# Performance work log

Measured on AMD Instinct MI355X. Metric: run time of the kernel, lower is better.

Reference implementation:

```python
import jax, jax.numpy as jnp
import numpy as np
import math

D_MODEL = 512
N_HEAD = 8
D_K = D_MODEL // N_HEAD
BN_EPS = 1e-5


def setup_inputs() -> dict:
    key = jax.random.key(0)
    ks = jax.random.split(key, 24)
    B, L = 4, 2048
    s = 0.02
    inp = {
        'query': jax.random.normal(ks[0], (B, L, D_MODEL), jnp.float32),
        'key':   jax.random.normal(ks[1], (B, L, D_MODEL), jnp.float32),
        'value': jax.random.normal(ks[2], (B, L, D_MODEL), jnp.float32),
        # multi-scale conv (kernel sizes 3 and 5)
        'conv_w3': jax.random.normal(ks[3], (D_MODEL, D_MODEL, 3), jnp.float32) * s,
        'conv_b3': jnp.zeros((D_MODEL,), jnp.float32),
        'conv_w5': jax.random.normal(ks[4], (D_MODEL, D_MODEL, 5), jnp.float32) * s,
        'conv_b5': jnp.zeros((D_MODEL,), jnp.float32),
        # batchnorm over 2*d_model channels (inference mode, running stats)
        'bn_gamma': jnp.ones((2 * D_MODEL,), jnp.float32),
        'bn_beta':  jnp.zeros((2 * D_MODEL,), jnp.float32),
        'bn_mean':  jnp.zeros((2 * D_MODEL,), jnp.float32),
        'bn_var':   jnp.ones((2 * D_MODEL,), jnp.float32),
        # linear projections (torch layout: [out, in])
        'wq':  jax.random.normal(ks[5], (D_MODEL, D_MODEL), jnp.float32) * s,
        'bq':  jnp.zeros((D_MODEL,), jnp.float32),
        'wkl': jax.random.normal(ks[6], (D_MODEL, 2 * D_MODEL), jnp.float32) * s,
        'bkl': jnp.zeros((D_MODEL,), jnp.float32),
        'wkg': jax.random.normal(ks[7], (D_MODEL, D_MODEL), jnp.float32) * s,
        'bkg': jnp.zeros((D_MODEL,), jnp.float32),
        'wv':  jax.random.normal(ks[8], (D_MODEL, D_MODEL), jnp.float32) * s,
        'bv':  jnp.zeros((D_MODEL,), jnp.float32),
        'wo':  jax.random.normal(ks[9], (D_MODEL, D_MODEL), jnp.float32) * s,
        'bo':  jnp.zeros((D_MODEL,), jnp.float32),
    }
    return inp


def _conv1d_same(x_ncl, w_oik, b, pad):
    # x: [B, C_in, L], w: [C_out, C_in, K]
    y = jax.lax.conv_general_dilated(
        x_ncl, w_oik, window_strides=(1,), padding=[(pad, pad)],
        dimension_numbers=('NCH', 'OIH', 'NCH'))
    return y + b[None, :, None]


def _heads(x, B, L):
    # [B, L, D] -> [B, L, H, d_k]
    return x.reshape(B, L, N_HEAD, D_K)


def reference(query, key, value, conv_w3, conv_b3, conv_w5, conv_b5,
              bn_gamma, bn_beta, bn_mean, bn_var,
              wq, bq, wkl, bkl, wkg, bkg, wv, bv, wo, bo):
    B, L, _ = query.shape
    # local key path: multi-scale conv over sequence dim
    k_ncl = key.transpose(0, 2, 1)                      # [B, D, L]
    c3 = _conv1d_same(k_ncl, conv_w3, conv_b3, 1)       # [B, D, L]
    c5 = _conv1d_same(k_ncl, conv_w5, conv_b5, 2)       # [B, D, L]
    cat = jnp.concatenate([c3, c5], axis=1)             # [B, 2D, L]
    bn = (cat - bn_mean[None, :, None]) * (bn_gamma[None, :, None]
          * jax.lax.rsqrt(bn_var[None, :, None] + BN_EPS)) + bn_beta[None, :, None]
    key_local = bn.transpose(0, 2, 1)                   # [B, L, 2D]

    q  = _heads(query @ wq.T + bq, B, L)                # [B, L, H, dk]
    kl = _heads(key_local @ wkl.T + bkl, B, L)
    kg = _heads(key @ wkg.T + bkg, B, L)
    v  = _heads(value @ wv.T + bv, B, L)

    scale = 1.0 / math.sqrt(D_K)
    s_loc = jnp.einsum('bqhd,bkhd->bhqk', q, kl) * scale
    s_glo = jnp.einsum('bqhd,bkhd->bhqk', q, kg) * scale
    a_loc = jax.nn.softmax(s_loc, axis=-1)
    a_glo = jax.nn.softmax(s_glo, axis=-1)
    x = jnp.einsum('bhqk,bkhd->bqhd', a_loc, v) + jnp.einsum('bhqk,bkhd->bqhd', a_glo, v)
    x = x.reshape(B, L, N_HEAD * D_K)
    return x @ wo.T + bo
```

## Files before the change

### kernel.cpp

```cpp
#include <hip/hip_runtime.h>
#include <hip/hip_bf16.h>

#define D_MODEL 512
#define SEQ_L   2048
#define NBATCH  4
#define BLROWS  8192
#define BN_EPS_F 1e-5f
#define QK_SCALE 0.18033688011112042f

typedef __attribute__((ext_vector_type(8))) short bf16x8;
typedef __attribute__((ext_vector_type(4))) float f32x4;
typedef __attribute__((ext_vector_type(16))) float f32x16;
typedef __attribute__((ext_vector_type(2))) int i32x2;

__device__ __forceinline__ unsigned short f2bf(float f){
  union { float f; unsigned u; } x; x.f = f;
  return (unsigned short)((x.u + 0x7fffu + ((x.u >> 16) & 1u)) >> 16);
}
__device__ __forceinline__ unsigned pack2bf(float a, float b){
  return (unsigned)f2bf(a) | ((unsigned)f2bf(b) << 16);
}
__device__ __forceinline__ unsigned cvt_pk(float a, float b){
  unsigned r;
  asm("v_cvt_pk_bf16_f32 %0, %1, %2" : "=v"(r) : "v"(a), "v"(b));
  return r;
}
__device__ __forceinline__ float exp2fast(float x){
  float r;
  asm("v_exp_f32 %0, %1" : "=v"(r) : "v"(x));
  return r;
}
__device__ __forceinline__ f32x4 mfma16(bf16x8 a, bf16x8 b, f32x4 c){
  return __builtin_amdgcn_mfma_f32_16x16x32_bf16(a, b, c, 0, 0, 0);
}
__device__ __forceinline__ f32x16 mfma32(bf16x8 a, bf16x8 b, f32x16 c){
  return __builtin_amdgcn_mfma_f32_32x32x16_bf16(a, b, c, 0, 0, 0);
}
__device__ __forceinline__ bf16x8 ldb8(const unsigned short* p){
  return *reinterpret_cast<const bf16x8*>(p);
}
__device__ __forceinline__ void gld16(const void* g, void* l){
  __builtin_amdgcn_global_load_lds(
      (const __attribute__((address_space(1))) unsigned*)g,
      (__attribute__((address_space(3))) unsigned*)l, 16, 0, 0);
}

__global__ void k_prep(
    const float* __restrict__ query, const float* __restrict__ key,
    const float* __restrict__ value,
    const float* __restrict__ wq, const float* __restrict__ wkg,
    const float* __restrict__ wv, const float* __restrict__ wo,
    const float* __restrict__ wkl, const float* __restrict__ gamma,
    const float* __restrict__ beta, const float* __restrict__ mean,
    const float* __restrict__ var, const float* __restrict__ cb3,
    const float* __restrict__ cb5, const float* __restrict__ w3,
    const float* __restrict__ w5, const float* __restrict__ bkl,
    unsigned short* __restrict__ qb, unsigned short* __restrict__ kb,
    unsigned short* __restrict__ vb,
    unsigned short* __restrict__ wqb, unsigned short* __restrict__ wkgb,
    unsigned short* __restrict__ wvb, unsigned short* __restrict__ wob,
    unsigned short* __restrict__ Acat, unsigned short* __restrict__ Bcat,
    float* __restrict__ beff, unsigned short* __restrict__ zeros)
{
  const int blk = blockIdx.x, tid = threadIdx.x;
  if (blk < 12288){
    const int z = blk >> 12, bb = blk & 4095;
    const float* s = (z == 0) ? query : (z == 1) ? key : value;
    unsigned short* d = (z == 0) ? qb : (z == 1) ? kb : vb;
    int i = (bb * 256 + tid) * 4;
    float4 v = *reinterpret_cast<const float4*>(s + i);
    uint2 o; o.x = pack2bf(v.x, v.y); o.y = pack2bf(v.z, v.w);
    *reinterpret_cast<uint2*>(d + i) = o;
  } else if (blk < 13312){
    const int r = blk - 12288, z = r >> 8, bb = r & 255;
    const float* s = (z == 0) ? wq : (z == 1) ? wkg : (z == 2) ? wv : wo;
    unsigned short* d = (z == 0) ? wqb : (z == 1) ? wkgb : (z == 2) ? wvb : wob;
    const float sc = (z == 0) ? QK_SCALE : 1.f;
    int i = (bb * 256 + tid) * 4;
    float4 v = *reinterpret_cast<const float4*>(s + i);
    uint2 o; o.x = pack2bf(v.x * sc, v.y * sc); o.y = pack2bf(v.z * sc, v.w * sc);
    *reinterpret_cast<uint2*>(d + i) = o;
  } else if (blk < 13824){
    int base = (blk - 13312) * 1024 + tid * 4;
    ushort4 out;
#pragma unroll
    for (int j = 0; j < 4; ++j){
      int idx = base + j;
      int o = idx >> 10, ch = idx & 1023;
      int c = (ch < 512) ? (512 + ch) : (ch - 512);
      float a = gamma[c] * rsqrtf(var[c] + BN_EPS_F);
      ((unsigned short*)&out)[j] = f2bf(wkl[o * 1024 + c] * a);
    }
    *reinterpret_cast<ushort4*>(Acat + base) = out;
  } else if (blk < 16384){
    int base = (blk - 13824) * 1024 + tid * 4;
    ushort4 out;
#pragma unroll
    for (int j = 0; j < 4; ++j){
      int idx = base + j;
      int t = idx >> 19; int r = idx & 524287;
      int ci = r >> 10, ch = r & 1023;
      float v;
      if (ch < 512) v = w5[ch * 2560 + ci * 5 + t];
      else {
        int c3 = ch - 512;
        v = (t >= 1 && t <= 3) ? w3[c3 * 1536 + ci * 3 + (t - 1)] : 0.0f;
      }
      ((unsigned short*)&out)[j] = f2bf(v);
    }
    *reinterpret_cast<ushort4*>(Bcat + base) = out;
  } else if (blk < 16512){
    const int o = (blk - 16384) * 4 + (tid >> 6);
    const int lane = tid & 63;
    float acc = 0.f;
    for (int c = lane; c < 1024; c += 64){
      float a = gamma[c] * rsqrtf(var[c] + BN_EPS_F);
      float cb = (c < 512) ? cb3[c] : cb5[c - 512];
      acc += wkl[o * 1024 + c] * (a * cb + beta[c] - a * mean[c]);
    }
#pragma unroll
    for (int off = 32; off; off >>= 1) acc += __shfl_down(acc, off);
    if (lane == 0) beff[o] = acc + bkl[o];
  } else {
    if (tid < 128) zeros[tid] = 0;
  }
}

template<int MODE, int BN = 128>
__global__ __launch_bounds__(256, 2) void k_gemm(
    const unsigned short* __restrict__ A, const unsigned short* __restrict__ Bm,
    void* __restrict__ Cp, const float* __restrict__ bias, float bias_scale,
    int M, int N, int K, int lda, int ldb, int ldc,
    long sAz, long sBz, long sCz)
{
  __shared__ unsigned short As[128 * 64];
  __shared__ unsigned short Bs[BN * 64];
  constexpr int NW2 = BN / 32;
  const int m0 = blockIdx.x * 128, n0 = blockIdx.y * BN;
  const unsigned short* Az = A + (long)blockIdx.z * sAz;
  const unsigned short* Bz = Bm + (long)blockIdx.z * sBz;
  const int tid = threadIdx.x, wid = tid >> 6, lane = tid & 63;
  const int l15 = lane & 15, hq = lane >> 4;
  const int wr = wid >> 1, wc = wid & 1;
  f32x4 acc[4][NW2];
#pragma unroll
  for (int m = 0; m < 4; ++m)
#pragma unroll
    for (int n = 0; n < NW2; ++n) acc[m][n] = f32x4{0.f, 0.f, 0.f, 0.f};
  const int nkt = K >> 6;
  const int wv4 = wid * 512;
  const int srow = tid >> 3;
  const int scol = (tid & 7) * 8;
  for (int kt = 0; kt < nkt; ++kt){
    __syncthreads();
    const int k0 = kt << 6;
#pragma unroll
    for (int i = 0; i < 4; ++i){
      int row = srow + i * 32;
      gld16(Az + (long)(m0 + row) * lda + k0 + scol, As + i * 2048 + wv4);
    }
#pragma unroll
    for (int i = 0; i < BN / 32; ++i){
      int row = srow + i * 32;
      gld16(Bz + (long)(n0 + row) * ldb + k0 + scol, Bs + i * 2048 + wv4);
    }
    __syncthreads();
#pragma unroll
    for (int ks = 0; ks < 2; ++ks){
      const int kb_ = ks * 32 + 8 * hq;
      bf16x8 af[4], bfr[NW2];
#pragma unroll
      for (int m = 0; m < 4; ++m) af[m] = ldb8(As + (wr * 64 + m * 16 + l15) * 64 + kb_);
#pragma unroll
      for (int n = 0; n < NW2; ++n)
        bfr[n] = ldb8(Bs + (wc * (BN / 2) + n * 16 + l15) * 64 + kb_);
#pragma unroll
      for (int m = 0; m < 4; ++m)
#pragma unroll
        for (int n = 0; n < NW2; ++n) acc[m][n] = mfma16(af[m], bfr[n], acc[m][n]);
    }
  }
  const int crow0 = m0 + wr * 64, ccol0 = n0 + wc * (BN / 2);
#pragma unroll
  for (int n = 0; n < NW2; ++n){
    int col = ccol0 + n * 16 + l15;
    float bv = bias ? bias[col] * bias_scale : 0.f;
#pragma unroll
    for (int m = 0; m < 4; ++m){
      int rowb = crow0 + m * 16 + 4 * hq;
#pragma unroll
      for (int r = 0; r < 4; ++r){
        float v = acc[m][n][r] + bv;
        long off = (long)(rowb + r) * ldc + col + (long)blockIdx.z * sCz;
        if (MODE == 1) ((float*)Cp)[off] = v;
        else ((unsigned short*)Cp)[off] = f2bf(v);
      }
    }
  }
}

__global__ __launch_bounds__(256, 2) void k_gemm4(
    const unsigned short* __restrict__ qb, const unsigned short* __restrict__ kb,
    const unsigned short* __restrict__ vb,
    const unsigned short* __restrict__ wqb, const unsigned short* __restrict__ wkgb,
    const unsigned short* __restrict__ wvb, const unsigned short* __restrict__ Weff,
    const float* __restrict__ bq, const float* __restrict__ bkg,
    const float* __restrict__ bv_, const float* __restrict__ beff,
    unsigned short* __restrict__ Qm, unsigned short* __restrict__ KGm,
    unsigned short* __restrict__ Vt, unsigned short* __restrict__ KLm,
    const unsigned short* __restrict__ zeros)
{
  __shared__ unsigned short Asb[128 * 64 + 64 * 64];
  unsigned short* As = Asb;
  unsigned short* Bs = Asb + 128 * 64;
  const int z = blockIdx.z;
  const int m0 = blockIdx.x * 128, n0 = blockIdx.y * 64;
  const unsigned short* A = (z == 1) ? qb : (z == 3) ? vb : kb;
  const unsigned short* B = (z == 0) ? Weff : (z == 1) ? wqb : (z == 2) ? wkgb : wvb;
  const float* bias = (z == 0) ? beff : (z == 1) ? bq : (z == 2) ? bkg : bv_;
  const float bs = (z == 1) ? QK_SCALE : 1.f;
  const int nkt = (z == 0) ? 40 : 8;
  const int tid = threadIdx.x, wid = tid >> 6, lane = tid & 63;
  const int l15 = lane & 15, hq = lane >> 4;
  const int wr = wid >> 1, wc = wid & 1;
  f32x4 acc[4][2];
#pragma unroll
  for (int m = 0; m < 4; ++m){ acc[m][0] = f32x4{0.f,0.f,0.f,0.f}; acc[m][1] = f32x4{0.f,0.f,0.f,0.f}; }
  const int wv4 = wid * 512;
  const int srow = tid >> 3;
  const int scol = (tid & 7) * 8;
  for (int kt = 0; kt < nkt; ++kt){
    __syncthreads();
    if (z == 0){
      const int t = kt >> 3; const int ci0 = (kt & 7) << 6;
#pragma unroll
      for (int i = 0; i < 4; ++i){
        int row = srow + i * 32;
        int gr = m0 + row;
        int sl = (gr & (SEQ_L - 1)) + t - 2;
        const unsigned short* sp = ((unsigned)sl < (unsigned)SEQ_L)
            ? (A + (long)(gr + t - 2) * D_MODEL + ci0 + scol) : (zeros + scol);
        gld16(sp, As + i * 2048 + wv4);
      }
#pragma unroll
      for (int i = 0; i < 2; ++i){
        int row = srow + i * 32;
        gld16(B + (long)t * 262144 + (long)(n0 + row) * D_MODEL + ci0 + scol,
              Bs + i * 2048 + wv4);
      }
    } else {
      const int k0 = kt << 6;
#pragma unroll
      for (int i = 0; i < 4; ++i){
        int row = srow + i * 32;
        gld16(A + (long)(m0 + row) * D_MODEL + k0 + scol, As + i * 2048 + wv4);
      }
#pragma unroll
      for (int i = 0; i < 2; ++i){
        int row = srow + i * 32;
        gld16(B + (long)(n0 + row) * D_MODEL + k0 + scol, Bs + i * 2048 + wv4);
      }
    }
    __syncthreads();
#pragma unroll
    for (int ks = 0; ks < 2; ++ks){
      const int kb_ = ks * 32 + 8 * hq;
      bf16x8 af[4], bfr[2];
#pragma unroll
      for (int m = 0; m < 4; ++m) af[m] = ldb8(As + (wr * 64 + m * 16 + l15) * 64 + kb_);
      bfr[0] = ldb8(Bs + (wc * 32 + l15) * 64 + kb_);
      bfr[1] = ldb8(Bs + (wc * 32 + 16 + l15) * 64 + kb_);
#pragma unroll
      for (int m = 0; m < 4; ++m){
        acc[m][0] = mfma16(af[m], bfr[0], acc[m][0]);
        acc[m][1] = mfma16(af[m], bfr[1], acc[m][1]);
      }
    }
  }
  if (z == 3){
    __syncthreads();
    unsigned short* T = Asb;
#pragma unroll
    for (int n = 0; n < 2; ++n){
      int lcol = wc * 32 + n * 16 + l15;
      float bvv = bv_[n0 + lcol];
#pragma unroll
      for (int m = 0; m < 4; ++m){
        int lrow = wr * 64 + m * 16 + 4 * hq;
        union { unsigned short s[4]; unsigned long long u; } pk4;
#pragma unroll
        for (int r = 0; r < 4; ++r) pk4.s[r] = f2bf(acc[m][n][r] + bvv);
        *reinterpret_cast<unsigned long long*>(T + lcol * 136 + lrow) = pk4.u;
      }
    }
    __syncthreads();
    const int bq_ = m0 >> 11;
    const long vtbase = ((long)(bq_ << 9) + n0) * SEQ_L + (m0 & (SEQ_L - 1));
#pragma unroll
    for (int i = 0; i < 4; ++i){
      int idx = tid + i * 256;
      int d = idx >> 4, lc = idx & 15;
      bf16x8 v = ldb8(T + d * 136 + lc * 8);
      *reinterpret_cast<bf16x8*>(Vt + vtbase + (long)d * SEQ_L + lc * 8) = v;
    }
    return;
  }
  unsigned short* C = (z == 0) ? KLm : (z == 1) ? Qm : KGm;
  const int crow0 = m0 + wr * 64, ccol0 = n0 + wc * 32;
#pragma unroll
  for (int n = 0; n < 2; ++n){
    int col = ccol0 + n * 16 + l15;
    float bvv = bias[col] * bs;
#pragma unroll
    for (int m = 0; m < 4; ++m){
      int rowb = crow0 + m * 16 + 4 * hq;
#pragma unroll
      for (int r = 0; r < 4; ++r)
        C[(long)(rowb + r) * D_MODEL + col] = f2bf(acc[m][n][r] + bvv);
    }
  }
}

__global__ __launch_bounds__(512, 2) void k_attn(
    const unsigned short* __restrict__ Q, const unsigned short* __restrict__ KLp,
    const unsigned short* __restrict__ KGp, const unsigned short* __restrict__ Vt,
    unsigned short* __restrict__ X)
{
  __shared__ unsigned short smem[6][4096];

  const int lin = blockIdx.x + (blockIdx.y << 4);
  const int sw  = ((lin & 7) << 6) + (lin >> 3);
  const int qi = sw & 15, bh = sw >> 4;
  const int b = bh >> 3, hb = (bh & 7) << 6;
  const int tid = threadIdx.x, wid = tid >> 6, lane = tid & 63;
  const int path = wid >> 2, wg = wid & 3;
  const int l31 = lane & 31, hi = lane >> 5;
  const int s7 = l31 & 7;
  const int q0 = qi * 128 + wg * 32;
  const long rb = (long)b * SEQ_L;

  const long qrow = (rb + q0 + l31) * D_MODEL + hb + hi * 8;
  bf16x8 qf[4];
#pragma unroll
  for (int ch = 0; ch < 4; ++ch) qf[ch] = ldb8(Q + qrow + ch * 16);

  f32x16 o[2];
  o[0] = 0.f; o[1] = 0.f;
  float srun = 0.f;

  auto stage = [&](const unsigned short* gbase, long rowstride, unsigned short* lb){
    const int idx0 = wid * 64;
    const int idx = idx0 + lane;
    const int row = idx >> 3, cl = idx & 7;
    const int cg = cl ^ (row & 7);
    gld16(gbase + (long)row * rowstride + cg * 8, lb + idx0 * 8);
  };

  const unsigned short* klg = KLp + rb * D_MODEL + hb;
  const unsigned short* kgg = KGp + rb * D_MODEL + hb;
  const unsigned short* vtg = Vt + ((long)b * D_MODEL + hb) * SEQ_L;

  stage(klg, D_MODEL, smem[0]);
  stage(kgg, D_MODEL, smem[2]);
  stage(vtg, SEQ_L,  smem[4]);
  asm volatile("s_waitcnt vmcnt(0)" ::: "memory");
  __syncthreads();

  int cur = 0;
#pragma unroll 1
  for (int t = 0; t < SEQ_L / 64; ++t){
    const int nxt = cur ^ 1;
    if (t < SEQ_L / 64 - 1){
      const long kvn = (long)(t + 1) * 64;
      stage(klg + kvn * D_MODEL, D_MODEL, smem[nxt]);
      stage(kgg + kvn * D_MODEL, D_MODEL, smem[2 + nxt]);
      stage(vtg + kvn,           SEQ_L,   smem[4 + nxt]);
    }
    const unsigned short* Kb_ = path ? smem[2 + cur] : smem[cur];
    const unsigned short* Vb_ = smem[4 + cur];
    f32x16 sa = 0.f, sb = 0.f;
    __builtin_amdgcn_s_setprio(1);
#pragma unroll
    for (int ch = 0; ch < 4; ++ch){
      bf16x8 k0 = ldb8(Kb_ + l31 * 64 + (((hi + 2 * ch) ^ s7) * 8));
      bf16x8 k1 = ldb8(Kb_ + (l31 + 32) * 64 + (((hi + 2 * ch) ^ s7) * 8));
      sa = mfma32(k0, qf[ch], sa);
      sb = mfma32(k1, qf[ch], sb);
    }
    __builtin_amdgcn_s_setprio(0);
#pragma unroll
    for (int r = 0; r < 16; ++r) sa[r] = exp2fast(sa[r]);
#pragma unroll
    for (int r = 0; r < 16; ++r) sb[r] = exp2fast(sb[r]);
    float w[8];
#pragma unroll
    for (int r = 0; r < 8; ++r) w[r] = (sa[r] + sa[r + 8]) + (sb[r] + sb[r + 8]);
    float sum = ((w[0] + w[1]) + (w[2] + w[3])) + ((w[4] + w[5]) + (w[6] + w[7]));
    i32x2 sr = __builtin_amdgcn_permlane32_swap(__float_as_int(sum), __float_as_int(sum), false, false);
    srun += __int_as_float(sr[0]) + __int_as_float(sr[1]);
    unsigned uu[2][4][2];
#pragma unroll
    for (int r4 = 0; r4 < 4; ++r4){
      uu[0][r4][0] = cvt_pk(sa[r4 * 4 + 0], sa[r4 * 4 + 1]);
      uu[0][r4][1] = cvt_pk(sa[r4 * 4 + 2], sa[r4 * 4 + 3]);
      uu[1][r4][0] = cvt_pk(sb[r4 * 4 + 0], sb[r4 * 4 + 1]);
      uu[1][r4][1] = cvt_pk(sb[r4 * 4 + 2], sb[r4 * 4 + 3]);
    }
    __builtin_amdgcn_s_setprio(1);
#pragma unroll
    for (int kc = 0; kc < 4; ++kc){
      const int tt = kc >> 1, kk = kc & 1;
      i32x2 rA = __builtin_amdgcn_permlane32_swap((int)uu[tt][2 * kk][0], (int)uu[tt][2 * kk + 1][0], false, false);
      i32x2 rB = __builtin_amdgcn_permlane32_swap((int)uu[tt][2 * kk][1], (int)uu[tt][2 * kk + 1][1], false, false);
      union { bf16x8 v; int w_[4]; } pb;
      pb.w_[0] = rA[0]; pb.w_[1] = rB[0]; pb.w_[2] = rA[1]; pb.w_[3] = rB[1];
      bf16x8 v0 = ldb8(Vb_ + l31 * 64 + (((kc * 2 + hi) ^ s7) * 8));
      bf16x8 v1 = ldb8(Vb_ + (l31 + 32) * 64 + (((kc * 2 + hi) ^ s7) * 8));
      o[0] = mfma32(v0, pb.v, o[0]);
      o[1] = mfma32(v1, pb.v, o[1]);
    }
    __builtin_amdgcn_s_setprio(0);
    asm volatile("s_waitcnt vmcnt(0)" ::: "memory");
    __syncthreads();
    cur = nxt;
  }

  float* shF = (float*)smem;
  const int mb = (wg * 64 + lane) * 32;
  const float inv = 1.f / srun;
  if (path){
#pragma unroll
    for (int r = 0; r < 16; ++r){
      shF[mb + r]      = o[0][r] * inv;
      shF[mb + 16 + r] = o[1][r] * inv;
    }
  }
  __syncthreads();
  if (!path){
    const long xrow = (rb + q0 + l31) * D_MODEL + hb + hi * 4;
#pragma unroll
    for (int dt = 0; dt < 2; ++dt)
#pragma unroll
      for (int r4 = 0; r4 < 4; ++r4){
        float v0 = o[dt][r4 * 4 + 0] * inv + shF[mb + dt * 16 + r4 * 4 + 0];
        float v1 = o[dt][r4 * 4 + 1] * inv + shF[mb + dt * 16 + r4 * 4 + 1];
        float v2 = o[dt][r4 * 4 + 2] * inv + shF[mb + dt * 16 + r4 * 4 + 2];
        float v3 = o[dt][r4 * 4 + 3] * inv + shF[mb + dt * 16 + r4 * 4 + 3];
        uint2 pk2; pk2.x = cvt_pk(v0, v1); pk2.y = cvt_pk(v2, v3);
        *reinterpret_cast<uint2*>(X + xrow + dt * 32 + r4 * 8) = pk2;
      }
  }
}

extern "C" void kernel_launch(void* const* d_in, const int* in_sizes, int n_in,
                              void* d_out, int out_size, void* d_ws, size_t ws_size,
                              hipStream_t stream)
{
  const float* query = (const float*)d_in[0];
  const float* key   = (const float*)d_in[1];
  const float* value = (const float*)d_in[2];
  const float* w3    = (const float*)d_in[3];
  const float* cb3   = (const float*)d_in[4];
  const float* w5    = (const float*)d_in[5];
  const float* cb5   = (const float*)d_in[6];
  const float* gamma = (const float*)d_in[7];
  const float* beta  = (const float*)d_in[8];
  const float* mean  = (const float*)d_in[9];
  const float* var   = (const float*)d_in[10];
  const float* wq    = (const float*)d_in[11];
  const float* bq    = (const float*)d_in[12];
  const float* wkl   = (const float*)d_in[13];
  const float* bkl   = (const float*)d_in[14];
  const float* wkg   = (const float*)d_in[15];
  const float* bkg   = (const float*)d_in[16];
  const float* wv    = (const float*)d_in[17];
  const float* bv    = (const float*)d_in[18];
  const float* wo    = (const float*)d_in[19];
  const float* bo    = (const float*)d_in[20];

  char* ws = (char*)d_ws;
  const size_t MB = 1024 * 1024;
  unsigned short* qb   = (unsigned short*)(ws + 0 * MB);
  unsigned short* kb   = (unsigned short*)(ws + 8 * MB);
  unsigned short* vb   = (unsigned short*)(ws + 16 * MB);
  unsigned short* Qm   = (unsigned short*)(ws + 24 * MB);
  unsigned short* KGm  = (unsigned short*)(ws + 32 * MB);
  unsigned short* Vt   = (unsigned short*)(ws + 40 * MB);
  unsigned short* KLm  = (unsigned short*)(ws + 48 * MB);
  unsigned short* Xm   = vb;
  unsigned short* Bcat = Qm;
  unsigned short* Acat = KGm;
  unsigned short* Weff = (unsigned short*)(ws + 56 * MB);
  unsigned short* wqb  = (unsigned short*)(ws + 56 * MB + 2621440);
  unsigned short* wkgb = wqb + 262144;
  unsigned short* wvb  = wqb + 524288;
  unsigned short* wob  = wqb + 786432;
  float*          beff = (float*)(ws + 61 * MB);
  unsigned short* zeros= (unsigned short*)(ws + 61 * MB + 4096);

  k_prep<<<16513, 256, 0, stream>>>(query, key, value, wq, wkg, wv, wo,
      wkl, gamma, beta, mean, var, cb3, cb5, w3, w5, bkl,
      qb, kb, vb, wqb, wkgb, wvb, wob, Acat, Bcat, beff, zeros);

  k_gemm<0, 64><<<dim3(4, 8, 5), 256, 0, stream>>>(Acat, Bcat, Weff, nullptr, 0.f,
      512, 512, 1024, 1024, 1024, 512, 0L, 524288L, 262144L);

  k_gemm4<<<dim3(64, 8, 4), 256, 0, stream>>>(qb, kb, vb, wqb, wkgb, wvb, Weff,
      bq, bkg, bv, beff, Qm, KGm, Vt, KLm, zeros);

  k_attn<<<dim3(16, 32), dim3(512), 0, stream>>>(Qm, KLm, KGm, Vt, Xm);

  k_gemm<1, 64><<<dim3(64, 8), 256, 0, stream>>>(Xm, wob, d_out, bo, 1.f,
      BLROWS, D_MODEL, D_MODEL, D_MODEL, D_MODEL, D_MODEL, 0L, 0L, 0L);
}
```

Before: 201.6 us.

## Double-buffer LDS tiles in projection GEMM kernels to overlap loads with MFMA

Both GEMM kernels (k_gemm and the fused four-way projection k_gemm4) now use two LDS buffers. The next K-tile is issued with async global-to-LDS loads before computing on the current tile, so load latency overlaps with MFMA work, and each iteration ends with one waitcnt and barrier instead of two barriers. This doubles LDS use per block, which may limit occupancy under the two-blocks-per-CU launch bound.

```diff
diff --git a/kernel.cpp b/kernel.cpp
--- a/kernel.cpp
+++ b/kernel.cpp
@@ -133,8 +133,8 @@
     int M, int N, int K, int lda, int ldb, int ldc,
     long sAz, long sBz, long sCz)
 {
-  __shared__ unsigned short As[128 * 64];
-  __shared__ unsigned short Bs[BN * 64];
+  __shared__ unsigned short As[2][128 * 64];
+  __shared__ unsigned short Bs[2][BN * 64];
   constexpr int NW2 = BN / 32;
   const int m0 = blockIdx.x * 128, n0 = blockIdx.y * BN;
   const unsigned short* Az = A + (long)blockIdx.z * sAz;
@@ -151,34 +151,43 @@
   const int wv4 = wid * 512;
   const int srow = tid >> 3;
   const int scol = (tid & 7) * 8;
-  for (int kt = 0; kt < nkt; ++kt){
-    __syncthreads();
+
+  auto stg = [&](int kt, int bufi){
     const int k0 = kt << 6;
 #pragma unroll
     for (int i = 0; i < 4; ++i){
       int row = srow + i * 32;
-      gld16(Az + (long)(m0 + row) * lda + k0 + scol, As + i * 2048 + wv4);
+      gld16(Az + (long)(m0 + row) * lda + k0 + scol, As[bufi] + i * 2048 + wv4);
     }
 #pragma unroll
     for (int i = 0; i < BN / 32; ++i){
       int row = srow + i * 32;
-      gld16(Bz + (long)(n0 + row) * ldb + k0 + scol, Bs + i * 2048 + wv4);
-    }
-    __syncthreads();
+      gld16(Bz + (long)(n0 + row) * ldb + k0 + scol, Bs[bufi] + i * 2048 + wv4);
+    }
+  };
+
+  stg(0, 0);
+  asm volatile("s_waitcnt vmcnt(0)" ::: "memory");
+  __syncthreads();
+  for (int kt = 0; kt < nkt; ++kt){
+    const int cb = kt & 1;
+    if (kt + 1 < nkt) stg(kt + 1, cb ^ 1);
 #pragma unroll
     for (int ks = 0; ks < 2; ++ks){
       const int kb_ = ks * 32 + 8 * hq;
       bf16x8 af[4], bfr[NW2];
 #pragma unroll
-      for (int m = 0; m < 4; ++m) af[m] = ldb8(As + (wr * 64 + m * 16 + l15) * 64 + kb_);
+      for (int m = 0; m < 4; ++m) af[m] = ldb8(As[cb] + (wr * 64 + m * 16 + l15) * 64 + kb_);
 #pragma unroll
       for (int n = 0; n < NW2; ++n)
-        bfr[n] = ldb8(Bs + (wc * (BN / 2) + n * 16 + l15) * 64 + kb_);
+        bfr[n] = ldb8(Bs[cb] + (wc * (BN / 2) + n * 16 + l15) * 64 + kb_);
 #pragma unroll
       for (int m = 0; m < 4; ++m)
 #pragma unroll
         for (int n = 0; n < NW2; ++n) acc[m][n] = mfma16(af[m], bfr[n], acc[m][n]);
     }
+    asm volatile("s_waitcnt vmcnt(0)" ::: "memory");
+    __syncthreads();
   }
   const int crow0 = m0 + wr * 64, ccol0 = n0 + wc * (BN / 2);
 #pragma unroll
@@ -210,9 +219,7 @@
     unsigned short* __restrict__ Vt, unsigned short* __restrict__ KLm,
     const unsigned short* __restrict__ zeros)
 {
-  __shared__ unsigned short Asb[128 * 64 + 64 * 64];
-  unsigned short* As = Asb;
-  unsigned short* Bs = Asb + 128 * 64;
+  __shared__ unsigned short Asb[2][128 * 64 + 64 * 64];
   const int z = blockIdx.z;
   const int m0 = blockIdx.x * 128, n0 = blockIdx.y * 64;
   const unsigned short* A = (z == 1) ? qb : (z == 3) ? vb : kb;
@@ -229,8 +236,10 @@
   const int wv4 = wid * 512;
   const int srow = tid >> 3;
   const int scol = (tid & 7) * 8;
-  for (int kt = 0; kt < nkt; ++kt){
-    __syncthreads();
+
+  auto stg = [&](int kt, int bufi){
+    unsigned short* Asx = Asb[bufi];
+    unsigned short* Bsx = Asb[bufi] + 8192;
     if (z == 0){
       const int t = kt >> 3; const int ci0 = (kt & 7) << 6;
 #pragma unroll
@@ -240,46 +249,56 @@
         int sl = (gr & (SEQ_L - 1)) + t - 2;
         const unsigned short* sp = ((unsigned)sl < (unsigned)SEQ_L)
             ? (A + (long)(gr + t - 2) * D_MODEL + ci0 + scol) : (zeros + scol);
-        gld16(sp, As + i * 2048 + wv4);
+        gld16(sp, Asx + i * 2048 + wv4);
       }
 #pragma unroll
       for (int i = 0; i < 2; ++i){
         int row = srow + i * 32;
         gld16(B + (long)t * 262144 + (long)(n0 + row) * D_MODEL + ci0 + scol,
-              Bs + i * 2048 + wv4);
+              Bsx + i * 2048 + wv4);
       }
     } else {
       const int k0 = kt << 6;
 #pragma unroll
       for (int i = 0; i < 4; ++i){
         int row = srow + i * 32;
-        gld16(A + (long)(m0 + row) * D_MODEL + k0 + scol, As + i * 2048 + wv4);
+        gld16(A + (long)(m0 + row) * D_MODEL + k0 + scol, Asx + i * 2048 + wv4);
       }
 #pragma unroll
       for (int i = 0; i < 2; ++i){
         int row = srow + i * 32;
-        gld16(B + (long)(n0 + row) * D_MODEL + k0 + scol, Bs + i * 2048 + wv4);
-      }
-    }
-    __syncthreads();
+        gld16(B + (long)(n0 + row) * D_MODEL + k0 + scol, Bsx + i * 2048 + wv4);
+      }
+    }
+  };
+
+  stg(0, 0);
+  asm volatile("s_waitcnt vmcnt(0)" ::: "memory");
+  __syncthreads();
+  for (int kt = 0; kt < nkt; ++kt){
+    const int cb = kt & 1;
+    if (kt + 1 < nkt) stg(kt + 1, cb ^ 1);
+    const unsigned short* Asx = Asb[cb];
+    const unsigned short* Bsx = Asb[cb] + 8192;
 #pragma unroll
     for (int ks = 0; ks < 2; ++ks){
       const int kb_ = ks * 32 + 8 * hq;
       bf16x8 af[4], bfr[2];
 #pragma unroll
-      for (int m = 0; m < 4; ++m) af[m] = ldb8(As + (wr * 64 + m * 16 + l15) * 64 + kb_);
-      bfr[0] = ldb8(Bs + (wc * 32 + l15) * 64 + kb_);
-      bfr[1] = ldb8(Bs + (wc * 32 + 16 + l15) * 64 + kb_);
+      for (int m = 0; m < 4; ++m) af[m] = ldb8(Asx + (wr * 64 + m * 16 + l15) * 64 + kb_);
+      bfr[0] = ldb8(Bsx + (wc * 32 + l15) * 64 + kb_);
+      bfr[1] = ldb8(Bsx + (wc * 32 + 16 + l15) * 64 + kb_);
 #pragma unroll
       for (int m = 0; m < 4; ++m){
         acc[m][0] = mfma16(af[m], bfr[0], acc[m][0]);
         acc[m][1] = mfma16(af[m], bfr[1], acc[m][1]);
       }
     }
+    asm volatile("s_waitcnt vmcnt(0)" ::: "memory");
+    __syncthreads();
   }
   if (z == 3){
-    __syncthreads();
-    unsigned short* T = Asb;
+    unsigned short* T = Asb[0];
 #pragma unroll
     for (int n = 0; n < 2; ++n){
       int lcol = wc * 32 + n * 16 + l15;
```

Result: slower. 207.4 us (+2.9%).
